# Kernel tuning notes

Measured on AMD Instinct MI355X. Metric: run time of the kernel, lower is better.

Reference implementation:

```python
import jax, jax.numpy as jnp
import numpy as np
from jax import lax

B_, T_, E_, H_, V_ = 8, 128, 256, 512, 32000


def setup_inputs() -> dict:
    key = jax.random.key(0)
    ks = jax.random.split(key, 16)
    s = 0.05
    n = lambda k, shp: (jax.random.normal(k, shp, dtype=jnp.float32) * s)
    return {
        "tokens": jax.random.randint(ks[0], (B_, T_), 0, V_),
        "TASK": 0,
        "embed_table": n(ks[1], (V_, E_)),
        # shared LSTM (PyTorch gate order i,f,g,o packed along 4H)
        "Wih_s": n(ks[2], (E_, 4 * H_)),
        "Whh_s": n(ks[3], (H_, 4 * H_)),
        "b_s": n(ks[4], (4 * H_,)),
        # task attention projections
        "Ws_w": n(ks[5], (E_ + 2 * H_, H_)),
        "Ws_b": n(ks[6], (H_,)),
        "Us_w": n(ks[7], (H_, 1)),
        "Us_b": n(ks[8], (1,)),
        # task-specific message LSTM cell (extra message path Rt)
        "Wih_t": n(ks[9], (E_, 4 * H_)),
        "Whh_t": n(ks[10], (H_, 4 * H_)),
        "Wmh_t": n(ks[11], (H_, 4 * H_)),
        "b_t": n(ks[12], (4 * H_,)),
    }


def _gates(pre, c):
    i, f, g, o = jnp.split(pre, 4, axis=-1)
    c_new = jax.nn.sigmoid(f) * c + jax.nn.sigmoid(i) * jnp.tanh(g)
    h_new = jax.nn.sigmoid(o) * jnp.tanh(c_new)
    return h_new, c_new


def _forward(tokens, TASK, embed_table, Wih_s, Whh_s, b_s,
             Ws_w, Ws_b, Us_w, Us_b, Wih_t, Whh_t, Wmh_t, b_t):
    B, T = tokens.shape
    H = Whh_s.shape[0]
    emb = embed_table[tokens]                     # [B,T,E]
    emb_t = jnp.transpose(emb, (1, 0, 2))         # [T,B,E]
    zeros = jnp.zeros((B, H), dtype=emb.dtype)

    # shared single-layer LSTM over time
    def shared_cell(carry, x_t):
        h, c = carry
        h, c = _gates(x_t @ Wih_s + h @ Whh_s + b_s, c)
        return (h, c), h

    (h_last, _), shared_out_t = lax.scan(shared_cell, (zeros, zeros), emb_t)
    shared_out = jnp.transpose(shared_out_t, (1, 0, 2))   # [B,T,H]
    h_shared = h_last[:, None, :]                         # [B,1,H]

    # task-specific attention-weighted message LSTM
    def task_step(carry, x_t):
        h, c = carry
        h_task = jnp.broadcast_to(h[:, None, :], (B, T, H))
        catted = jnp.concatenate([shared_out, h_task, emb], axis=-1)  # [B,T,E+2H]
        a = jnp.tanh(catted @ Ws_w + Ws_b)                            # [B,T,H]
        Si = a @ Us_w + Us_b                                          # [B,T,1]
        Bw = jax.nn.softmax(Si, axis=1)                               # over time
        Rt = jnp.sum(Bw * h_shared, axis=1)                           # [B,H]
        h, c = _gates(x_t @ Wih_t + h @ Whh_t + Rt @ Wmh_t + b_t, c)
        return (h, c), h

    _, outs_t = lax.scan(task_step, (zeros, zeros), emb_t)
    return jnp.transpose(outs_t, (1, 0, 2))               # [B,T,H]


def reference(tokens, TASK, embed_table, Wih_s, Whh_s, b_s,
              Ws_w, Ws_b, Us_w, Us_b, Wih_t, Whh_t, Wmh_t, b_t):
    return _forward(tokens, TASK, embed_table, Wih_s, Whh_s, b_s,
                    Ws_w, Ws_b, Us_w, Us_b, Wih_t, Whh_t, Wmh_t, b_t)
```

## Files before the change

### kernel.cpp

```cpp
#include <hip/hip_runtime.h>
#include <math.h>

#define B_   8
#define T_   128
#define E_   256
#define H_   512
#define G_   2048
#define NWG  256
#define NTHR 512
#define XP   130

typedef unsigned int u32;


__device__ __forceinline__ float sigf(float x) { return 1.0f / (1.0f + expf(-x)); }

__device__ __forceinline__ unsigned short f2bf(float x) {
  u32 u = __float_as_uint(x);
  u += 0x7fffu + ((u >> 16) & 1u);
  return (unsigned short)(u >> 16);
}
__device__ __forceinline__ float bf2f(unsigned short s) {
  return __uint_as_float(((u32)s) << 16);
}

__global__ void init_ws(u32* w) {
  int i = blockIdx.x * blockDim.x + threadIdx.x;
  if (i < 4096)      w[i] = 0u;
  else if (i < 8192) w[i] = 1u;
}

__device__ __forceinline__ void stage_W(const float* __restrict__ W, int rows,
                                        int s, float* __restrict__ Wl) {
  for (int idx = threadIdx.x; idx < rows * 64; idx += NTHR) {
    int k = idx >> 6, c = idx & 63;
    Wl[idx] = W[k * G_ + ((c >> 4) * H_ + s * 16 + (c & 15))];
  }
}

__attribute__((amdgpu_waves_per_eu(2)))
__global__ __launch_bounds__(NTHR, 1) void lstm_all(
    const int* __restrict__ tokens, const float* __restrict__ embed,
    const float* __restrict__ Wih_s, const float* __restrict__ Whh_s,
    const float* __restrict__ b_s,
    const float* __restrict__ Wih_t, const float* __restrict__ Whh_t,
    const float* __restrict__ Wmh_t, const float* __restrict__ b_t,
    float* __restrict__ out, u32* __restrict__ img) {
  __shared__ float Wl[H_ * 64];
  __shared__ unsigned short Xl[64 * XP];
  __shared__ float h_lds[H_];
  __shared__ float part[NTHR];

  const int tid = threadIdx.x;
  const int l   = tid & 63;
  const int wv  = tid >> 6;
  const int b   = blockIdx.x & 7;
  const int s   = blockIdx.x >> 3;
  const int p4  = l >> 4;

  float wreg[64];

  auto computeX = [&](const float* __restrict__ Wih, const float* __restrict__ bias) {
    stage_W(Wih, E_, s, Wl);
    __syncthreads();
    const int t = tid >> 2, grp = tid & 3;
    const int tok = tokens[b * T_ + t];
    const float4* er = (const float4*)(embed + (size_t)tok * E_);
    float acc[16];
#pragma unroll
    for (int j = 0; j < 16; ++j) acc[j] = bias[grp * H_ + s * 16 + j];
    for (int e4 = 0; e4 < E_ / 4; ++e4) {
      float4 em = er[e4];
#pragma unroll
      for (int eo = 0; eo < 4; ++eo) {
        float ev = reinterpret_cast<const float*>(&em)[eo];
        const float* wr = Wl + (e4 * 4 + eo) * 64 + grp * 16;
#pragma unroll
        for (int j = 0; j < 16; ++j) acc[j] += ev * wr[j];
      }
    }
#pragma unroll
    for (int j = 0; j < 16; ++j) Xl[(grp * 16 + j) * XP + t] = f2bf(acc[j]);
  };

  auto load_wreg = [&] {
#pragma unroll
    for (int kk = 0; kk < 64; ++kk) wreg[kk] = Wl[(wv * 64 + kk) * 64 + l];
#pragma unroll
    for (int kk = 0; kk < 64; ++kk) asm volatile("" : "+v"(wreg[kk]));
  };

  auto do_dot = [&]() -> float {
    float a0 = 0.f, a1 = 0.f, a2 = 0.f, a3 = 0.f;
    const float4* h4 = (const float4*)(h_lds + wv * 64);
#pragma unroll
    for (int kk = 0; kk < 16; ++kk) {
      float4 hv = h4[kk];
      a0 += hv.x * wreg[kk * 4 + 0];
      a1 += hv.y * wreg[kk * 4 + 1];
      a2 += hv.z * wreg[kk * 4 + 2];
      a3 += hv.w * wreg[kk * 4 + 3];
    }
    return (a0 + a1) + (a2 + a3);
  };

  auto poll_stage = [&](unsigned gen) {
    const u32 par = (gen >> 1) & 1u;
    const u32* src = img + (gen & 1u) * 4096 + b * H_ + tid;
    u32 u;
    while (((u = __hip_atomic_load(src, __ATOMIC_RELAXED,
                                   __HIP_MEMORY_SCOPE_AGENT)) & 1u) != par)
      __builtin_amdgcn_s_sleep(1);
    h_lds[tid] = __uint_as_float(u);
  };

  computeX(Wih_s, b_s);
  __syncthreads();
  stage_W(Whh_s, H_, s, Wl);
  __syncthreads();
  load_wreg();

  float c_reg = 0.f, Mreg = 0.f;

  for (int t = 0; t < T_; ++t) {
    if (t > 0) poll_stage((unsigned)t);
    __syncthreads();
    part[tid] = (t > 0) ? do_dot() : 0.f;
    __syncthreads();
    if (wv == 0) {
      float sum = 0.f;
#pragma unroll
      for (int q = 0; q < 8; ++q) sum += part[q * 64 + l];
      float pre = sum + bf2f(Xl[l * XP + t]);
      float v16 = __shfl_xor(pre, 16), v32 = __shfl_xor(pre, 32), v48 = __shfl_xor(pre, 48);
      auto pick = [&](int m) { int x = p4 ^ m; return x == 0 ? pre : (x == 1 ? v16 : (x == 2 ? v32 : v48)); };
      float gi = pick(0), gf = pick(1), gg = pick(2), go = pick(3);
      float cn = sigf(gf) * c_reg + sigf(gi) * tanhf(gg);
      float hn = sigf(go) * tanhf(cn);
      c_reg = cn;
      const unsigned gw = (unsigned)t + 1u;
      if (p4 == 0) {
        u32 hb = (__float_as_uint(hn) & ~1u) | ((gw >> 1) & 1u);
        __hip_atomic_store(img + (gw & 1u) * 4096 + b * H_ + s * 16 + l, hb,
                           __ATOMIC_RELAXED, __HIP_MEMORY_SCOPE_AGENT);
      }
    }
  }

  __syncthreads();
  stage_W(Wmh_t, H_, s, Wl);
  __syncthreads();
  load_wreg();
  poll_stage(128u);
  __syncthreads();
  part[tid] = do_dot();
  __syncthreads();
  if (wv == 0) {
    float sum = 0.f;
#pragma unroll
    for (int q = 0; q < 8; ++q) sum += part[q * 64 + l];
    Mreg = sum;
  }

  __syncthreads();
  computeX(Wih_t, b_t);
  __syncthreads();
  stage_W(Whh_t, H_, s, Wl);
  __syncthreads();
  load_wreg();

  c_reg = 0.f;
  for (int t = 0; t < T_; ++t) {
    if (t > 0) poll_stage(128u + (unsigned)t);
    __syncthreads();
    part[tid] = (t > 0) ? do_dot() : 0.f;
    __syncthreads();
    if (wv == 0) {
      float sum = 0.f;
#pragma unroll
      for (int q = 0; q < 8; ++q) sum += part[q * 64 + l];
      float pre = sum + bf2f(Xl[l * XP + t]) + Mreg;
      float v16 = __shfl_xor(pre, 16), v32 = __shfl_xor(pre, 32), v48 = __shfl_xor(pre, 48);
      auto pick = [&](int m) { int x = p4 ^ m; return x == 0 ? pre : (x == 1 ? v16 : (x == 2 ? v32 : v48)); };
      float gi = pick(0), gf = pick(1), gg = pick(2), go = pick(3);
      float cn = sigf(gf) * c_reg + sigf(gi) * tanhf(gg);
      float hn = sigf(go) * tanhf(cn);
      c_reg = cn;
      if (p4 == 0) {
        out[b * (T_ * H_) + t * H_ + s * 16 + l] = hn;
        if (t < T_ - 1) {
          const unsigned gw = 129u + (unsigned)t;
          u32 hb = (__float_as_uint(hn) & ~1u) | ((gw >> 1) & 1u);
          __hip_atomic_store(img + (gw & 1u) * 4096 + b * H_ + s * 16 + l, hb,
                             __ATOMIC_RELAXED, __HIP_MEMORY_SCOPE_AGENT);
        }
      }
    }
  }
}

extern "C" void kernel_launch(void* const* d_in, const int* in_sizes, int n_in,
                              void* d_out, int out_size, void* d_ws, size_t ws_size,
                              hipStream_t stream) {
  const int*   tokens = (const int*)d_in[0];
  const float* embed  = (const float*)d_in[2];
  const float* Wih_s  = (const float*)d_in[3];
  const float* Whh_s  = (const float*)d_in[4];
  const float* b_s    = (const float*)d_in[5];
  const float* Wih_t  = (const float*)d_in[10];
  const float* Whh_t  = (const float*)d_in[11];
  const float* Wmh_t  = (const float*)d_in[12];
  const float* b_t    = (const float*)d_in[13];
  float* out = (float*)d_out;
  u32*   img = (u32*)d_ws;

  hipLaunchKernelGGL(init_ws, dim3(8), dim3(1024), 0, stream, img);
  hipLaunchKernelGGL(lstm_all, dim3(NWG), dim3(NTHR), 0, stream,
                     tokens, embed, Wih_s, Whh_s, b_s,
                     Wih_t, Whh_t, Wmh_t, b_t, out, img);
}
```

Measured before the change: 758.6 us.

## Make each wave own its own gate columns and drop per-step block barriers

Reorganizes the recurrent matvec so each wave computes the full K=512 reduction for two hidden units (8 gate columns). Each lane polls 8 hidden values directly from global memory with 64-bit atomic loads, and the partial sums are reduced with cross-lane shuffles. This removes the LDS staging of h, the partial-sum array, and two __syncthreads per timestep, so all waves run the gate math instead of only wave 0. The weight layout in LDS and in computeX is permuted to match. The cost is more global polling traffic per lane and more shuffle work per step.

Measured after the change: 2.478 ms. 227% more time.

```diff
diff --git a/kernel.cpp b/kernel.cpp
--- a/kernel.cpp
+++ b/kernel.cpp
@@ -11,6 +11,7 @@
 #define XP   130
 
 typedef unsigned int u32;
+typedef unsigned long long u64;
 
 
 __device__ __forceinline__ float sigf(float x) { return 1.0f / (1.0f + expf(-x)); }
@@ -34,7 +35,8 @@
                                         int s, float* __restrict__ Wl) {
   for (int idx = threadIdx.x; idx < rows * 64; idx += NTHR) {
     int k = idx >> 6, c = idx & 63;
-    Wl[idx] = W[k * G_ + ((c >> 4) * H_ + s * 16 + (c & 15))];
+    int wv = c >> 3, g = (c >> 1) & 3, u = c & 1;
+    Wl[idx] = W[k * G_ + g * H_ + s * 16 + wv * 2 + u];
   }
 }
 
@@ -48,17 +50,99 @@
     float* __restrict__ out, u32* __restrict__ img) {
   __shared__ float Wl[H_ * 64];
   __shared__ unsigned short Xl[64 * XP];
-  __shared__ float h_lds[H_];
-  __shared__ float part[NTHR];
 
   const int tid = threadIdx.x;
   const int l   = tid & 63;
   const int wv  = tid >> 6;
   const int b   = blockIdx.x & 7;
   const int s   = blockIdx.x >> 3;
-  const int p4  = l >> 4;
+
+  const int c8  = ((l & 1) << 2) | (l & 2) | ((l >> 2) & 1);
+  const int g_  = c8 >> 1, u_ = c8 & 1;
+  const int xcol = g_ * 16 + wv * 2 + u_;
+  auto mmap = [](int x) { return ((x & 1) << 2) | (x & 2) | ((x >> 2) & 1); };
+  const int base8 = l & ~7;
+  const int sg0 = base8 | mmap(0 + u_);
+  const int sg1 = base8 | mmap(2 + u_);
+  const int sg2 = base8 | mmap(4 + u_);
+  const int sg3 = base8 | mmap(6 + u_);
+  const bool st = (l == 0) || (l == 4);
+  const int jcol = s * 16 + wv * 2 + (l >> 2);
 
   float wreg[64];
+
+  auto load_wreg = [&]() {
+#pragma unroll
+    for (int kk = 0; kk < 8; ++kk) {
+      const float4* p = (const float4*)(Wl + (l * 8 + kk) * 64 + wv * 8);
+      float4 a = p[0], q = p[1];
+      wreg[kk * 8 + 0] = a.x; wreg[kk * 8 + 1] = a.y;
+      wreg[kk * 8 + 2] = a.z; wreg[kk * 8 + 3] = a.w;
+      wreg[kk * 8 + 4] = q.x; wreg[kk * 8 + 5] = q.y;
+      wreg[kk * 8 + 6] = q.z; wreg[kk * 8 + 7] = q.w;
+    }
+#pragma unroll
+    for (int i = 0; i < 64; ++i) asm volatile("" : "+v"(wreg[i]));
+  };
+
+  auto rec_dot = [&](unsigned gen) -> float {
+    const u32 par = (gen >> 1) & 1u;
+    const u64* src = (const u64*)(img + (size_t)(gen & 1u) * 4096 + b * H_)
+                     + (size_t)l * 4;
+    u64 v0;
+    for (;;) {
+      v0 = __hip_atomic_load(src, __ATOMIC_RELAXED, __HIP_MEMORY_SCOPE_AGENT);
+      if (!((((u32)v0 ^ par) | ((u32)(v0 >> 32) ^ par)) & 1u)) break;
+      __builtin_amdgcn_s_sleep(1);
+    }
+    u64 v1, v2, v3;
+    for (;;) {
+      v1 = __hip_atomic_load(src + 1, __ATOMIC_RELAXED, __HIP_MEMORY_SCOPE_AGENT);
+      v2 = __hip_atomic_load(src + 2, __ATOMIC_RELAXED, __HIP_MEMORY_SCOPE_AGENT);
+      v3 = __hip_atomic_load(src + 3, __ATOMIC_RELAXED, __HIP_MEMORY_SCOPE_AGENT);
+      u32 bad = ((u32)v1 ^ par) | ((u32)(v1 >> 32) ^ par) |
+                ((u32)v2 ^ par) | ((u32)(v2 >> 32) ^ par) |
+                ((u32)v3 ^ par) | ((u32)(v3 >> 32) ^ par);
+      if (!(bad & 1u)) break;
+      __builtin_amdgcn_s_sleep(1);
+    }
+    float h8[8];
+    h8[0] = __uint_as_float((u32)v0); h8[1] = __uint_as_float((u32)(v0 >> 32));
+    h8[2] = __uint_as_float((u32)v1); h8[3] = __uint_as_float((u32)(v1 >> 32));
+    h8[4] = __uint_as_float((u32)v2); h8[5] = __uint_as_float((u32)(v2 >> 32));
+    h8[6] = __uint_as_float((u32)v3); h8[7] = __uint_as_float((u32)(v3 >> 32));
+
+    float acc[8];
+#pragma unroll
+    for (int c = 0; c < 8; ++c) acc[c] = 0.0f;
+#pragma unroll
+    for (int kk = 0; kk < 8; ++kk) {
+      float hv = h8[kk];
+#pragma unroll
+      for (int c = 0; c < 8; ++c) acc[c] += hv * wreg[kk * 8 + c];
+    }
+    float o4[4];
+#pragma unroll
+    for (int j = 0; j < 4; ++j) {
+      float send = (l & 1) ? acc[j] : acc[4 + j];
+      float keep = (l & 1) ? acc[4 + j] : acc[j];
+      o4[j] = keep + __shfl_xor(send, 1);
+    }
+    float o2[2];
+#pragma unroll
+    for (int j = 0; j < 2; ++j) {
+      float send = (l & 2) ? o4[j] : o4[2 + j];
+      float keep = (l & 2) ? o4[2 + j] : o4[j];
+      o2[j] = keep + __shfl_xor(send, 2);
+    }
+    float send = (l & 4) ? o2[0] : o2[1];
+    float keep = (l & 4) ? o2[1] : o2[0];
+    float sum = keep + __shfl_xor(send, 4);
+    sum += __shfl_xor(sum, 8);
+    sum += __shfl_xor(sum, 16);
+    sum += __shfl_xor(sum, 32);
+    return sum;
+  };
 
   auto computeX = [&](const float* __restrict__ Wih, const float* __restrict__ bias) {
     stage_W(Wih, E_, s, Wl);
@@ -74,44 +158,23 @@
 #pragma unroll
       for (int eo = 0; eo < 4; ++eo) {
         float ev = reinterpret_cast<const float*>(&em)[eo];
-        const float* wr = Wl + (e4 * 4 + eo) * 64 + grp * 16;
-#pragma unroll
-        for (int j = 0; j < 16; ++j) acc[j] += ev * wr[j];
+        const float* wr = Wl + (e4 * 4 + eo) * 64;
+#pragma unroll
+        for (int j = 0; j < 16; ++j)
+          acc[j] += ev * wr[(j >> 1) * 8 + grp * 2 + (j & 1)];
       }
     }
 #pragma unroll
     for (int j = 0; j < 16; ++j) Xl[(grp * 16 + j) * XP + t] = f2bf(acc[j]);
   };
 
-  auto load_wreg = [&] {
-#pragma unroll
-    for (int kk = 0; kk < 64; ++kk) wreg[kk] = Wl[(wv * 64 + kk) * 64 + l];
-#pragma unroll
-    for (int kk = 0; kk < 64; ++kk) asm volatile("" : "+v"(wreg[kk]));
-  };
-
-  auto do_dot = [&]() -> float {
-    float a0 = 0.f, a1 = 0.f, a2 = 0.f, a3 = 0.f;
-    const float4* h4 = (const float4*)(h_lds + wv * 64);
-#pragma unroll
-    for (int kk = 0; kk < 16; ++kk) {
-      float4 hv = h4[kk];
-      a0 += hv.x * wreg[kk * 4 + 0];
-      a1 += hv.y * wreg[kk * 4 + 1];
-      a2 += hv.z * wreg[kk * 4 + 2];
-      a3 += hv.w * wreg[kk * 4 + 3];
-    }
-    return (a0 + a1) + (a2 + a3);
-  };
-
-  auto poll_stage = [&](unsigned gen) {
-    const u32 par = (gen >> 1) & 1u;
-    const u32* src = img + (gen & 1u) * 4096 + b * H_ + tid;
-    u32 u;
-    while (((u = __hip_atomic_load(src, __ATOMIC_RELAXED,
-                                   __HIP_MEMORY_SCOPE_AGENT)) & 1u) != par)
-      __builtin_amdgcn_s_sleep(1);
-    h_lds[tid] = __uint_as_float(u);
+  auto gates = [&](float pre, float& c_reg) -> float {
+    float pi = __shfl(pre, sg0), pf = __shfl(pre, sg1);
+    float pg = __shfl(pre, sg2), po = __shfl(pre, sg3);
+    float cn = sigf(pf) * c_reg + sigf(pi) * tanhf(pg);
+    float hn = sigf(po) * tanhf(cn);
+    c_reg = cn;
+    return hn;
   };
 
   computeX(Wih_s, b_s);
@@ -120,80 +183,44 @@
   __syncthreads();
   load_wreg();
 
-  float c_reg = 0.f, Mreg = 0.f;
-
+  float c_reg = 0.0f;
   for (int t = 0; t < T_; ++t) {
-    if (t > 0) poll_stage((unsigned)t);
-    __syncthreads();
-    part[tid] = (t > 0) ? do_dot() : 0.f;
-    __syncthreads();
-    if (wv == 0) {
-      float sum = 0.f;
-#pragma unroll
-      for (int q = 0; q < 8; ++q) sum += part[q * 64 + l];
-      float pre = sum + bf2f(Xl[l * XP + t]);
-      float v16 = __shfl_xor(pre, 16), v32 = __shfl_xor(pre, 32), v48 = __shfl_xor(pre, 48);
-      auto pick = [&](int m) { int x = p4 ^ m; return x == 0 ? pre : (x == 1 ? v16 : (x == 2 ? v32 : v48)); };
-      float gi = pick(0), gf = pick(1), gg = pick(2), go = pick(3);
-      float cn = sigf(gf) * c_reg + sigf(gi) * tanhf(gg);
-      float hn = sigf(go) * tanhf(cn);
-      c_reg = cn;
-      const unsigned gw = (unsigned)t + 1u;
-      if (p4 == 0) {
+    float S = (t > 0) ? rec_dot((unsigned)t) : 0.0f;
+    float pre = S + bf2f(Xl[xcol * XP + t]);
+    float hn = gates(pre, c_reg);
+    const unsigned gw = (unsigned)t + 1u;
+    if (st) {
+      u32 hb = (__float_as_uint(hn) & ~1u) | ((gw >> 1) & 1u);
+      __hip_atomic_store(img + (gw & 1u) * 4096 + b * H_ + jcol, hb,
+                         __ATOMIC_RELAXED, __HIP_MEMORY_SCOPE_AGENT);
+    }
+  }
+
+  __syncthreads();
+  stage_W(Wmh_t, H_, s, Wl);
+  __syncthreads();
+  load_wreg();
+  float Mreg = rec_dot(128u);
+
+  __syncthreads();
+  computeX(Wih_t, b_t);
+  __syncthreads();
+  stage_W(Whh_t, H_, s, Wl);
+  __syncthreads();
+  load_wreg();
+
+  c_reg = 0.0f;
+  for (int t = 0; t < T_; ++t) {
+    float S = (t > 0) ? rec_dot(128u + (unsigned)t) : 0.0f;
+    float pre = S + bf2f(Xl[xcol * XP + t]) + Mreg;
+    float hn = gates(pre, c_reg);
+    if (st) {
+      out[b * (T_ * H_) + t * H_ + jcol] = hn;
+      if (t < T_ - 1) {
+        const unsigned gw = 129u + (unsigned)t;
         u32 hb = (__float_as_uint(hn) & ~1u) | ((gw >> 1) & 1u);
-        __hip_atomic_store(img + (gw & 1u) * 4096 + b * H_ + s * 16 + l, hb,
+        __hip_atomic_store(img + (gw & 1u) * 4096 + b * H_ + jcol, hb,
                            __ATOMIC_RELAXED, __HIP_MEMORY_SCOPE_AGENT);
-      }
-    }
-  }
-
-  __syncthreads();
-  stage_W(Wmh_t, H_, s, Wl);
-  __syncthreads();
-  load_wreg();
-  poll_stage(128u);
-  __syncthreads();
-  part[tid] = do_dot();
-  __syncthreads();
-  if (wv == 0) {
-    float sum = 0.f;
-#pragma unroll
-    for (int q = 0; q < 8; ++q) sum += part[q * 64 + l];
-    Mreg = sum;
-  }
-
-  __syncthreads();
-  computeX(Wih_t, b_t);
-  __syncthreads();
-  stage_W(Whh_t, H_, s, Wl);
-  __syncthreads();
-  load_wreg();
-
-  c_reg = 0.f;
-  for (int t = 0; t < T_; ++t) {
-    if (t > 0) poll_stage(128u + (unsigned)t);
-    __syncthreads();
-    part[tid] = (t > 0) ? do_dot() : 0.f;
-    __syncthreads();
-    if (wv == 0) {
-      float sum = 0.f;
-#pragma unroll
-      for (int q = 0; q < 8; ++q) sum += part[q * 64 + l];
-      float pre = sum + bf2f(Xl[l * XP + t]) + Mreg;
-      float v16 = __shfl_xor(pre, 16), v32 = __shfl_xor(pre, 32), v48 = __shfl_xor(pre, 48);
-      auto pick = [&](int m) { int x = p4 ^ m; return x == 0 ? pre : (x == 1 ? v16 : (x == 2 ? v32 : v48)); };
-      float gi = pick(0), gf = pick(1), gg = pick(2), go = pick(3);
-      float cn = sigf(gf) * c_reg + sigf(gi) * tanhf(gg);
-      float hn = sigf(go) * tanhf(cn);
-      c_reg = cn;
-      if (p4 == 0) {
-        out[b * (T_ * H_) + t * H_ + s * 16 + l] = hn;
-        if (t < T_ - 1) {
-          const unsigned gw = 129u + (unsigned)t;
-          u32 hb = (__float_as_uint(hn) & ~1u) | ((gw >> 1) & 1u);
-          __hip_atomic_store(img + (gw & 1u) * 4096 + b * H_ + s * 16 + l, hb,
-                             __ATOMIC_RELAXED, __HIP_MEMORY_SCOPE_AGENT);
-        }
       }
     }
   }
```
